# Kernel optimization log

Hardware: AMD Instinct MI355X
Metric: run time of the kernel (lower is better)

Reference implementation:

```python
import jax, jax.numpy as jnp
import numpy as np

B, G, C = 32, 50, 80
IMG = 640
STRIDES = (8, 16, 32)
CENTER_RADIUS = 2.5


def _make_grids():
    xs, ys, ss = [], [], []
    for s in STRIDES:
        n = IMG // s
        yv, xv = np.meshgrid(np.arange(n, dtype=np.float32), np.arange(n, dtype=np.float32), indexing='ij')
        xs.append(xv.reshape(-1)); ys.append(yv.reshape(-1))
        ss.append(np.full(n * n, s, dtype=np.float32))
    return np.concatenate(xs), np.concatenate(ys), np.concatenate(ss)


def setup_inputs():
    xg, yg, sg = _make_grids()
    A = xg.shape[0]  # 8400
    ks = jax.random.split(jax.random.key(0), 5)
    # decoded box predictions near grid centers (cxcywh, pixel units)
    ctr = jnp.stack([jnp.asarray((xg + 0.5) * sg), jnp.asarray((yg + 0.5) * sg)], -1)[None] \
        + jax.random.normal(ks[0], (B, A, 2)) * 8.0
    wh = jnp.exp(jax.random.normal(ks[1], (B, A, 2)) * 0.5) * jnp.asarray(sg)[None, :, None] * 4.0
    pred_output = jnp.concatenate([ctr, wh, jax.random.normal(ks[2], (B, A, 1 + C))], -1)  # [B,A,85]
    obj_preds = jax.random.normal(ks[3], (B, A, 1))
    cls_preds = jax.random.normal(ks[4], (B, A, C))
    # labels [B,G,5] = (class, cx, cy, w, h); first num_gt rows valid, rest zero
    rng = np.random.RandomState(0)
    lab = np.zeros((B, G, 5), np.float32)
    for b in range(B):
        ng = rng.randint(5, G)
        lab[b, :ng, 0] = rng.randint(0, C, ng)
        lab[b, :ng, 1:3] = rng.uniform(40.0, IMG - 40.0, (ng, 2))
        lab[b, :ng, 3:5] = rng.uniform(20.0, 160.0, (ng, 2))
    return {"pred_output": pred_output, "obj_preds": obj_preds, "cls_preds": cls_preds,
            "labels": jnp.asarray(lab), "x_shifts": jnp.asarray(xg),
            "y_shifts": jnp.asarray(yg), "strides": jnp.asarray(sg)}


def _pairwise_iou_cxcywh(a, b):
    # a [G,4], b [A,4] -> [G,A]
    tl = jnp.maximum(a[:, None, :2] - a[:, None, 2:] * 0.5, b[None, :, :2] - b[None, :, 2:] * 0.5)
    br = jnp.minimum(a[:, None, :2] + a[:, None, 2:] * 0.5, b[None, :, :2] + b[None, :, 2:] * 0.5)
    area_a = a[:, 2] * a[:, 3]
    area_b = b[:, 2] * b[:, 3]
    en = jnp.all(tl < br, -1).astype(a.dtype)
    area_i = jnp.prod(br - tl, -1) * en
    return area_i / (area_a[:, None] + area_b[None, :] - area_i + 1e-16)


def _assign_one(gt, gt_valid, boxes, cls_logit, obj_logit, xg, yg, sg):
    # SimOTA assignment for a single image, fully vectorized over [G,A].
    # gt [G,5], gt_valid [G], boxes [A,4], cls_logit [A,C], obj_logit [A,1]
    num_gt = gt.shape[0]
    gt_cls = gt[:, 0].astype(jnp.int32)
    gb = gt[:, 1:5]
    xc = (xg + 0.5) * sg
    yc = (yg + 0.5) * sg
    d_box = jnp.stack([
        xc[None, :] - (gb[:, 0:1] - gb[:, 2:3] * 0.5),
        (gb[:, 0:1] + gb[:, 2:3] * 0.5) - xc[None, :],
        yc[None, :] - (gb[:, 1:2] - gb[:, 3:4] * 0.5),
        (gb[:, 1:2] + gb[:, 3:4] * 0.5) - yc[None, :]], -1)
    in_boxes = (jnp.min(d_box, -1) > 0) & gt_valid[:, None]
    d_ctr = jnp.stack([
        xc[None, :] - (gb[:, 0:1] - CENTER_RADIUS * sg[None, :]),
        (gb[:, 0:1] + CENTER_RADIUS * sg[None, :]) - xc[None, :],
        yc[None, :] - (gb[:, 1:2] - CENTER_RADIUS * sg[None, :]),
        (gb[:, 1:2] + CENTER_RADIUS * sg[None, :]) - yc[None, :]], -1)
    in_ctr = (jnp.min(d_ctr, -1) > 0) & gt_valid[:, None]
    fg0 = jnp.any(in_boxes | in_ctr, 0)           # [A] candidate anchors (fg_mask)
    and_ctr = in_boxes & in_ctr                    # [G,A]
    ious = _pairwise_iou_cxcywh(gb, boxes) * fg0[None, :].astype(boxes.dtype) * gt_valid[:, None].astype(boxes.dtype)
    # pairwise BCE(sqrt(sig(cls)*sig(obj)), one_hot) summed over classes, without [G,A,C]
    logq = 0.5 * (jax.nn.log_sigmoid(cls_logit) + jax.nn.log_sigmoid(obj_logit))  # [A,C]
    q = jnp.clip(jnp.exp(logq), 1e-7, 1.0 - 1e-7)
    s_neg = jnp.sum(jnp.log1p(-q), -1)             # [A] sum_c log(1-q_c)
    q_gt = q[:, gt_cls].T                          # [G,A]
    cls_cost = -jnp.log(q_gt) + jnp.log1p(-q_gt) - s_neg[None, :]
    invalid = (~fg0)[None, :] | (~gt_valid)[:, None]
    cost = cls_cost - 3.0 * jnp.log(ious + 1e-8) + 1e5 * (~and_ctr) + 1e9 * invalid
    # dynamic-k: sum of top-10 ious per gt, truncated, min 1
    dyn_k = jnp.maximum(jnp.sum(jax.lax.top_k(ious, 10)[0], -1).astype(jnp.int32), 1)  # [G]
    ranks = jnp.argsort(jnp.argsort(cost, 1), 1)   # rank of each anchor in ascending cost
    matching = (ranks < dyn_k[:, None]) & gt_valid[:, None]
    # resolve anchors claimed by >1 gt: keep min-cost gt
    best_gt = jnp.argmin(cost, 0)                  # [A]
    onehot_best = jnp.arange(num_gt)[:, None] == best_gt[None, :]
    matching = jnp.where(jnp.sum(matching, 0)[None, :] > 1, onehot_best, matching)
    fg = jnp.any(matching, 0)                      # [A] final fg mask
    matched = jnp.argmax(matching, 0)              # [A] matched gt index
    pred_iou = jnp.sum(matching * ious, 0)         # [A]
    cls_t = jax.nn.one_hot(gt_cls[matched], cls_logit.shape[-1], dtype=boxes.dtype) \
        * (pred_iou * fg.astype(boxes.dtype))[:, None]
    return cls_t, fg, matched


def _forward(pred_output, obj_preds, cls_preds, labels, x_shifts, y_shifts, strides):
    bbox = pred_output[:, :, :4]
    gt_valid = labels.sum(-1) > 0
    cls_t, fg, matched = jax.vmap(_assign_one, in_axes=(0, 0, 0, 0, 0, None, None, None))(
        labels, gt_valid, bbox, cls_preds, obj_preds, x_shifts, y_shifts, strides)
    cls_t = jax.lax.stop_gradient(cls_t)  # get_assignments is @torch.no_grad()
    reg_t = jnp.take_along_axis(labels[:, :, 1:5], matched[:, :, None], axis=1)  # [B,A,4]
    fg_f = fg.astype(pred_output.dtype)
    num_fg = jnp.maximum(jnp.sum(fg_f), 1.0)
    # IoU loss (cxcywh), loss = 1 - iou^2, only on fg anchors
    tl = jnp.maximum(bbox[..., :2] - bbox[..., 2:] * 0.5, reg_t[..., :2] - reg_t[..., 2:] * 0.5)
    br = jnp.minimum(bbox[..., :2] + bbox[..., 2:] * 0.5, reg_t[..., :2] + reg_t[..., 2:] * 0.5)
    en = jnp.all(tl < br, -1).astype(bbox.dtype)
    area_i = jnp.prod(br - tl, -1) * en
    area_u = bbox[..., 2] * bbox[..., 3] + reg_t[..., 2] * reg_t[..., 3] - area_i
    iou = area_i / (area_u + 1e-16)
    loss_iou = jnp.sum((1.0 - iou ** 2) * fg_f) / num_fg
    bce = lambda x, y: jax.nn.softplus(x) - x * y  # BCEWithLogits, reduction='none'
    loss_obj = jnp.sum(bce(obj_preds[..., 0], fg_f)) / num_fg
    loss_cls = jnp.sum(bce(cls_preds, cls_t) * fg_f[..., None]) / num_fg
    return 5.0 * loss_iou + loss_obj + loss_cls


def reference(pred_output, obj_preds, cls_preds, labels, x_shifts, y_shifts, strides):
    return _forward(pred_output, obj_preds, cls_preds, labels, x_shifts, y_shifts, strides)
```

## Files before the change

### kernel.cpp

```cpp
#include <hip/hip_runtime.h>
#include <cstdint>
#include <cstddef>

#define BB 32
#define GG 50
#define CC 80
#define AA 8400
#define PCH (5 + CC)
#define NLB ((BB * AA + 255) / 256)
#define NXCD 8
#define FGBIT 63
#define SENTC 3.3e38f
#define SENTI 0x7fffffff

__device__ __forceinline__ float logsig_fast(float x) {
    float e = __expf(-fabsf(x));
    return fminf(x, 0.f) - __logf(1.f + e);
}
__device__ __forceinline__ void sp_ls(float x, float& sp, float& ls) {
    float e = __expf(-fabsf(x));
    float l = __logf(1.f + e);
    sp = fmaxf(x, 0.f) + l;
    ls = fminf(x, 0.f) - l;
}
__device__ __forceinline__ float softplusf(float x) {
    return fmaxf(x, 0.f) + log1pf(expf(-fabsf(x)));
}

__device__ __forceinline__ float pair_iou(float px, float py, float pw, float ph,
                                          float gx, float gy, float gw, float gh) {
    float tlx = fmaxf(gx - gw * 0.5f, px - pw * 0.5f);
    float tly = fmaxf(gy - gh * 0.5f, py - ph * 0.5f);
    float brx = fminf(gx + gw * 0.5f, px + pw * 0.5f);
    float bry = fminf(gy + gh * 0.5f, py + ph * 0.5f);
    float en = (tlx < brx && tly < bry) ? 1.f : 0.f;
    float ai = (brx - tlx) * (bry - tly) * en;
    return ai / (gw * gh + pw * ph - ai + 1e-16f);
}
__device__ __forceinline__ float cost_val(float x , float lo ,
                                          float sn , float v ,
                                          bool ac, bool f0, bool valid) {
    float lq = 0.5f * (logsig_fast(x) + lo);
    float q = fminf(fmaxf(__expf(lq), 1e-7f), 1.f - 1e-7f);
    float cst = -__logf(q) + __logf(1.f - q) - sn;
    cst -= 3.0f * __logf(v + 1e-8f);
    cst += 100000.0f * (ac ? 0.f : 1.f);
    cst += 1000000000.0f * ((!f0 || !valid) ? 1.f : 0.f);
    return cst;
}

__global__ __launch_bounds__(256)
void k_precompute(const float* __restrict__ pred, const float* __restrict__ obj,
                  const float* __restrict__ cls,
                  float2* __restrict__ lsn, float* __restrict__ sps,
                  float4* __restrict__ pbox) {
    int t = blockIdx.x * blockDim.x + threadIdx.x;
    int i = t >> 2;
    int sub = t & 3;
    if (i >= BB * AA) return;
    float lo = logsig_fast(obj[i]);
    const float4* c4 = (const float4*)(cls + (size_t)i * CC);
    float sn = 0.f, sp = 0.f;
#pragma unroll
    for (int j = 0; j < 5; j++) {
        float4 v = c4[sub + 4 * j];
        float xs4[4] = {v.x, v.y, v.z, v.w};
#pragma unroll
        for (int u = 0; u < 4; u++) {
            float x = xs4[u];
            float spx, lsx;
            sp_ls(x, spx, lsx);
            sp += spx;
            float q = __expf(0.5f * (lsx + lo));
            q = fminf(fmaxf(q, 1e-7f), 1.f - 1e-7f);
            sn += __logf(1.f - q);
        }
    }
    sp += __shfl_xor(sp, 1); sn += __shfl_xor(sn, 1);
    sp += __shfl_xor(sp, 2); sn += __shfl_xor(sn, 2);
    float pv = pred[(size_t)i * PCH + sub];
    ((float*)pbox)[(size_t)i * 4 + sub] = pv;
    if (sub == 0) {
        lsn[i] = make_float2(lo, sn);
        sps[i] = sp;
    }
}

__global__ void k_geom(const float* __restrict__ labels, const float* __restrict__ xs,
                       const float* __restrict__ ys, const float* __restrict__ ss,
                       unsigned long long* __restrict__ amask,
                       int* __restrict__ clist, int* __restrict__ ccnt) {
    int b = blockIdx.y;
    int a = blockIdx.x * blockDim.x + threadIdx.x;
    __shared__ float lab[GG * 5];
    __shared__ int lv[GG];
    for (int t = threadIdx.x; t < GG * 5; t += blockDim.x) lab[t] = labels[b * GG * 5 + t];
    __syncthreads();
    if (threadIdx.x < GG) {
        const float* r = lab + threadIdx.x * 5;
        lv[threadIdx.x] = ((r[0] + r[1] + r[2] + r[3] + r[4]) > 0.f) ? 1 : 0;
    }
    __syncthreads();
    if (a >= AA) return;
    float s = ss[a];
    float xc = (xs[a] + 0.5f) * s;
    float yc = (ys[a] + 0.5f) * s;
    unsigned long long m = 0;
    int any = 0;
    for (int g = 0; g < GG; g++) {
        if (!lv[g]) continue;
        const float* r = lab + g * 5;
        float gx = r[1], gy = r[2], gw = r[3], gh = r[4];
        float d1 = xc - (gx - gw * 0.5f);
        float d2 = (gx + gw * 0.5f) - xc;
        float d3 = yc - (gy - gh * 0.5f);
        float d4 = (gy + gh * 0.5f) - yc;
        bool ib = fminf(fminf(d1, d2), fminf(d3, d4)) > 0.f;
        float cr = 2.5f * s;
        float e1 = xc - (gx - cr);
        float e2 = (gx + cr) - xc;
        float e3 = yc - (gy - cr);
        float e4 = (gy + cr) - yc;
        bool ic = fminf(fminf(e1, e2), fminf(e3, e4)) > 0.f;
        if (ib || ic) any = 1;
        if (ib && ic) m |= 1ull << g;
    }
    if (any) m |= 1ull << FGBIT;
    amask[b * AA + a] = m;
    int lane = threadIdx.x & 63;
    unsigned long long act = __ballot(m != 0);
    if (act) {
        int leader = __ffsll(act) - 1;
        int base = 0;
        if (lane == leader) base = atomicAdd(&ccnt[b], __popcll(act));
        base = __shfl(base, leader);
        if (m != 0) {
            int off = __popcll(act & ((1ull << lane) - 1ull));
            clist[b * AA + base + off] = a;
        }
    }
}

__global__ __launch_bounds__(256)
void k_assign(const float4* __restrict__ pbox, const float2* __restrict__ lsn,
              const float* __restrict__ cls,
              const unsigned long long* __restrict__ amask,
              const float* __restrict__ labels,
              const int* __restrict__ clist, const int* __restrict__ ccnt,
              unsigned long long* __restrict__ mmask) {
    int bid = blockIdx.x;
    int w = (bid % NXCD) * (BB * GG / NXCD) + bid / NXCD;
    int b = w / GG, g = w % GG;
    const float* r = labels + (size_t)w * 5;
    float gcls = r[0], gx = r[1], gy = r[2], gw = r[3], gh = r[4];
    if (!((gcls + gx + gy + gw + gh) > 0.f)) return;
    int gtc = (int)gcls;
    int tid = threadIdx.x;
    int lane = tid & 63;
    int wv = tid >> 6;
    int cnt = ccnt[b];

    float ivl[10];
    float cvl[10];
    int   cil[10];
#pragma unroll
    for (int t = 0; t < 10; t++) { ivl[t] = 0.f; cvl[t] = SENTC; cil[t] = SENTI; }
    int nac = 0;

    for (int i0 = wv * 64; i0 < cnt; i0 += 256) {
        int i = i0 + lane;
        bool inr = i < cnt;
        int a = clist[b * AA + (inr ? i : (cnt - 1))];
        int ia = b * AA + a;
        unsigned long long am = amask[ia];
        float4 pb = pbox[ia];
        bool f0 = inr && ((am >> FGBIT) & 1ull);
        bool ac = inr && ((am >> g) & 1ull);
        nac += __popcll(__ballot(ac));
        float v = f0 ? pair_iou(pb.x, pb.y, pb.z, pb.w, gx, gy, gw, gh) : 0.f;
        {
            float mv = v;
            while (true) {
                unsigned long long mb = __ballot(mv > ivl[9]);
                if (!mb) break;
                int src = __ffsll(mb) - 1;
                float bv = __shfl(mv, src);
#pragma unroll
                for (int t = 0; t < 10; t++)
                    if (bv > ivl[t]) { float tmp = ivl[t]; ivl[t] = bv; bv = tmp; }
                if (lane == src) mv = -1.f;
            }
        }
        {
            float c = SENTC; int id = SENTI;
            if (ac) {
                float x = cls[(size_t)ia * CC + gtc];
                float2 ls = lsn[ia];
                c = cost_val(x, ls.x, ls.y, v, true, true, true);
                id = a;
            }
            while (true) {
                bool enter = (c < cvl[9]) || (c == cvl[9] && id < cil[9]);
                unsigned long long mb = __ballot(enter);
                if (!mb) break;
                int src = __ffsll(mb) - 1;
                float bc = __shfl(c, src);
                int bi = __shfl(id, src);
#pragma unroll
                for (int t = 0; t < 10; t++) {
                    bool sw = (bc < cvl[t]) || (bc == cvl[t] && bi < cil[t]);
                    if (sw) {
                        float tf = cvl[t]; cvl[t] = bc; bc = tf;
                        int ti = cil[t]; cil[t] = bi; bi = ti;
                    }
                }
                if (lane == src) { c = SENTC; id = SENTI; }
            }
        }
    }

    __shared__ float IV[4][10];
    __shared__ float CV[4][10];
    __shared__ int CI[4][10];
    __shared__ int NAC[4];
    __shared__ int s_k, s_n0;
    __shared__ int sel[10];

    if (lane == 0) {
#pragma unroll
        for (int t = 0; t < 10; t++) { IV[wv][t] = ivl[t]; CV[wv][t] = cvl[t]; CI[wv][t] = cil[t]; }
        NAC[wv] = nac;
    }
    __syncthreads();
    if (tid == 0) {
        int h[4] = {0, 0, 0, 0};
        float ssum = 0.f;
        for (int j = 0; j < 10; j++) {
            float bv = -1.f; int bc = 0;
#pragma unroll
            for (int c2 = 0; c2 < 4; c2++)
                if (h[c2] < 10 && IV[c2][h[c2]] > bv) { bv = IV[c2][h[c2]]; bc = c2; }
            ssum += bv;
            h[bc]++;
        }
        int k = (int)ssum;
        if (k < 1) k = 1;
        s_k = k;
        s_n0 = NAC[0] + NAC[1] + NAC[2] + NAC[3];
    }
    __syncthreads();
    int k = s_k;

    if (s_n0 < k) {
        const int chunk = AA / 4;
        int abase = wv * chunk, aend = abase + chunk;
#pragma unroll
        for (int t = 0; t < 10; t++) { cvl[t] = SENTC; cil[t] = SENTI; }
        for (int a0 = abase; a0 < aend; a0 += 64) {
            int a = a0 + lane;
            bool inr = a < aend;
            int ia = b * AA + (inr ? a : (aend - 1));
            unsigned long long am = amask[ia];
            bool f0 = inr && ((am >> FGBIT) & 1ull);
            bool ac = inr && ((am >> g) & 1ull);
            float v = 0.f;
            if (f0) {
                float4 pb = pbox[ia];
                v = pair_iou(pb.x, pb.y, pb.z, pb.w, gx, gy, gw, gh);
            }
            float c = SENTC; int id = SENTI;
            if (inr) {
                float x = cls[(size_t)ia * CC + gtc];
                float2 ls = lsn[ia];
                c = cost_val(x, ls.x, ls.y, v, ac, f0, true);
                id = a;
            }
            while (true) {
                bool enter = (c < cvl[9]) || (c == cvl[9] && id < cil[9]);
                unsigned long long mb = __ballot(enter);
                if (!mb) break;
                int src = __ffsll(mb) - 1;
                float bc = __shfl(c, src);
                int bi = __shfl(id, src);
#pragma unroll
                for (int t = 0; t < 10; t++) {
                    bool sw = (bc < cvl[t]) || (bc == cvl[t] && bi < cil[t]);
                    if (sw) {
                        float tf = cvl[t]; cvl[t] = bc; bc = tf;
                        int ti = cil[t]; cil[t] = bi; bi = ti;
                    }
                }
                if (lane == src) { c = SENTC; id = SENTI; }
            }
        }
        if (lane == 0) {
#pragma unroll
            for (int t = 0; t < 10; t++) { CV[wv][t] = cvl[t]; CI[wv][t] = cil[t]; }
        }
        __syncthreads();
    }

    if (tid == 0) {
        int h[4] = {0, 0, 0, 0};
        for (int j = 0; j < k; j++) {
            float bv = SENTC; int bix = SENTI; int bc = 0;
#pragma unroll
            for (int c2 = 0; c2 < 4; c2++) {
                if (h[c2] < 10) {
                    float av = CV[c2][h[c2]]; int ax = CI[c2][h[c2]];
                    if (av < bv || (av == bv && ax < bix)) { bv = av; bix = ax; bc = c2; }
                }
            }
            sel[j] = bix;
            h[bc]++;
        }
    }
    __syncthreads();
    if (tid < k) {
        atomicOr(&mmask[(size_t)b * AA + sel[tid]], 1ull << g);
    }
}

__global__ void k_loss(const float4* __restrict__ pbox, const float* __restrict__ obj,
                       const float* __restrict__ cls, const float* __restrict__ labels,
                       const float2* __restrict__ lsn,
                       const unsigned long long* __restrict__ amask,
                       const unsigned long long* __restrict__ mmask,
                       const float* __restrict__ sps, float* __restrict__ partial) {
    int i = blockIdx.x * blockDim.x + threadIdx.x;
    float li = 0.f, lo = 0.f, lc = 0.f, nf = 0.f;
    if (i < BB * AA) {
        int b = i / AA, a = i % AA;
        unsigned long long m = mmask[i];
        int cnt = __popcll(m);
        bool fg = (m != 0);
        int mg = 0;
        float4 pb = pbox[i];
        unsigned long long am = amask[i];
        bool f0 = (am >> FGBIT) & 1ull;
        if (cnt > 1) {
            float2 ls = lsn[i];
            float bv = 3.4e38f;
            for (int g = 0; g < GG; g++) {
                const float* r = labels + (size_t)(b * GG + g) * 5;
                float gcls = r[0], gx = r[1], gy = r[2], gw = r[3], gh = r[4];
                bool valid = (gcls + gx + gy + gw + gh) > 0.f;
                int gtc = (int)gcls;
                float raw = pair_iou(pb.x, pb.y, pb.z, pb.w, gx, gy, gw, gh);
                float v = raw * (f0 ? 1.f : 0.f) * (valid ? 1.f : 0.f);
                float x = cls[(size_t)i * CC + gtc];
                bool ac = (am >> g) & 1ull;
                float cst = cost_val(x, ls.x, ls.y, v, ac, f0, valid);
                if (cst < bv) { bv = cst; mg = g; }
            }
        } else if (cnt == 1) {
            mg = __ffsll((unsigned long long)m) - 1;
        }
        float o = obj[i];
        lo = softplusf(o) - (fg ? o : 0.f);
        if (fg) {
            const float* r = labels + (size_t)(b * GG + mg) * 5;
            float gcls = r[0], gx = r[1], gy = r[2], gw = r[3], gh = r[4];
            bool valid = (gcls + gx + gy + gw + gh) > 0.f;
            int gtc = (int)gcls;
            float piou = pair_iou(pb.x, pb.y, pb.z, pb.w, gx, gy, gw, gh)
                         * (f0 ? 1.f : 0.f) * (valid ? 1.f : 0.f);
            float tlx = fmaxf(pb.x - pb.z * 0.5f, gx - gw * 0.5f);
            float tly = fmaxf(pb.y - pb.w * 0.5f, gy - gh * 0.5f);
            float brx = fminf(pb.x + pb.z * 0.5f, gx + gw * 0.5f);
            float bry = fminf(pb.y + pb.w * 0.5f, gy + gh * 0.5f);
            float en = (tlx < brx && tly < bry) ? 1.f : 0.f;
            float ai = (brx - tlx) * (bry - tly) * en;
            float u = pb.z * pb.w + gw * gh - ai;
            float v2 = ai / (u + 1e-16f);
            li = 1.f - v2 * v2;
            lc = sps[i] - cls[(size_t)i * CC + gtc] * piou;
            nf = 1.f;
        }
    }
    for (int off = 32; off; off >>= 1) {
        li += __shfl_down(li, off);
        lo += __shfl_down(lo, off);
        lc += __shfl_down(lc, off);
        nf += __shfl_down(nf, off);
    }
    __shared__ float red[4][4];
    int wid = threadIdx.x >> 6;
    if ((threadIdx.x & 63) == 0) {
        red[wid][0] = li; red[wid][1] = lo; red[wid][2] = lc; red[wid][3] = nf;
    }
    __syncthreads();
    if (threadIdx.x == 0) {
        float s0 = 0.f, s1 = 0.f, s2 = 0.f, s3 = 0.f;
#pragma unroll
        for (int t = 0; t < 4; t++) {
            s0 += red[t][0]; s1 += red[t][1]; s2 += red[t][2]; s3 += red[t][3];
        }
        float4* pb = (float4*)partial;
        pb[blockIdx.x] = make_float4(s0, s1, s2, s3);
    }
}

__global__ void k_final(const float* __restrict__ partial, float* __restrict__ out) {
    int tid = threadIdx.x;
    float s0 = 0.f, s1 = 0.f, s2 = 0.f, s3 = 0.f;
    const float4* pb = (const float4*)partial;
    for (int i = tid; i < NLB; i += 256) {
        float4 v = pb[i];
        s0 += v.x; s1 += v.y; s2 += v.z; s3 += v.w;
    }
    for (int off = 32; off; off >>= 1) {
        s0 += __shfl_down(s0, off);
        s1 += __shfl_down(s1, off);
        s2 += __shfl_down(s2, off);
        s3 += __shfl_down(s3, off);
    }
    __shared__ float red[4][4];
    int wid = tid >> 6;
    if ((tid & 63) == 0) {
        red[wid][0] = s0; red[wid][1] = s1; red[wid][2] = s2; red[wid][3] = s3;
    }
    __syncthreads();
    if (tid == 0) {
        float li = 0.f, lo = 0.f, lc = 0.f, nf = 0.f;
#pragma unroll
        for (int t = 0; t < 4; t++) {
            li += red[t][0]; lo += red[t][1]; lc += red[t][2]; nf += red[t][3];
        }
        nf = fmaxf(nf, 1.f);
        out[0] = (5.f * li + lo + lc) / nf;
    }
}

extern "C" void kernel_launch(void* const* d_in, const int* in_sizes, int n_in,
                              void* d_out, int out_size, void* d_ws, size_t ws_size,
                              hipStream_t stream) {
    const float* pred = (const float*)d_in[0];
    const float* obj  = (const float*)d_in[1];
    const float* cls  = (const float*)d_in[2];
    const float* lab  = (const float*)d_in[3];
    const float* xs   = (const float*)d_in[4];
    const float* ys   = (const float*)d_in[5];
    const float* ss   = (const float*)d_in[6];
    float* out = (float*)d_out;

    const size_t BA = (size_t)BB * AA;

    float2* lsn  = (float2*)d_ws;
    float*  sps  = (float*)(lsn + BA);
    float4* pbox = (float4*)(sps + BA);
    unsigned long long* amask = (unsigned long long*)(pbox + BA);
    unsigned long long* mmask = amask + BA;
    float* partial = (float*)(mmask + BA);
    int* clist = (int*)(partial + (size_t)NLB * 4);
    int* ccnt  = clist + BA;

    hipMemsetAsync(mmask, 0, BA * sizeof(unsigned long long), stream);
    hipMemsetAsync(ccnt, 0, BB * sizeof(int), stream);

    dim3 blk(256);
    k_precompute<<<dim3((BB * AA * 4 + 255) / 256), blk, 0, stream>>>(pred, obj, cls,
                                                                      lsn, sps, pbox);
    k_geom<<<dim3((AA + 255) / 256, BB), blk, 0, stream>>>(lab, xs, ys, ss, amask,
                                                           clist, ccnt);
    k_assign<<<dim3(BB * GG), blk, 0, stream>>>(pbox, lsn, cls, amask, lab,
                                                clist, ccnt, mmask);
    k_loss<<<dim3(NLB), blk, 0, stream>>>(pbox, obj, cls, lab, lsn, amask,
                                          mmask, sps, partial);
    k_final<<<1, blk, 0, stream>>>(partial, out);
}
```

Measured before the change: 177.6 us.

## Replace per-element transcendental calls with product-of-terms logs in precompute

```diff
diff --git a/kernel.cpp b/kernel.cpp
--- a/kernel.cpp
+++ b/kernel.cpp
@@ -8,7 +8,6 @@
 #define AA 8400
 #define PCH (5 + CC)
 #define NLB ((BB * AA + 255) / 256)
-#define NXCD 8
 #define FGBIT 63
 #define SENTC 3.3e38f
 #define SENTI 0x7fffffff
@@ -16,12 +15,6 @@
 __device__ __forceinline__ float logsig_fast(float x) {
     float e = __expf(-fabsf(x));
     return fminf(x, 0.f) - __logf(1.f + e);
-}
-__device__ __forceinline__ void sp_ls(float x, float& sp, float& ls) {
-    float e = __expf(-fabsf(x));
-    float l = __logf(1.f + e);
-    sp = fmaxf(x, 0.f) + l;
-    ls = fminf(x, 0.f) - l;
 }
 __device__ __forceinline__ float softplusf(float x) {
     return fmaxf(x, 0.f) + log1pf(expf(-fabsf(x)));
@@ -59,23 +52,29 @@
     int sub = t & 3;
     if (i >= BB * AA) return;
     float lo = logsig_fast(obj[i]);
+    float K = __expf(0.5f * lo);
     const float4* c4 = (const float4*)(cls + (size_t)i * CC);
-    float sn = 0.f, sp = 0.f;
+    float smax = 0.f, psp = 1.f, p1 = 1.f, p2 = 1.f;
 #pragma unroll
     for (int j = 0; j < 5; j++) {
         float4 v = c4[sub + 4 * j];
         float xs4[4] = {v.x, v.y, v.z, v.w};
+        float pg = 1.f;
 #pragma unroll
         for (int u = 0; u < 4; u++) {
             float x = xs4[u];
-            float spx, lsx;
-            sp_ls(x, spx, lsx);
-            sp += spx;
-            float q = __expf(0.5f * (lsx + lo));
-            q = fminf(fmaxf(q, 1e-7f), 1.f - 1e-7f);
-            sn += __logf(1.f - q);
-        }
-    }
+            float th = __expf(-0.5f * fabsf(x));
+            float t2 = th * th;
+            smax += fmaxf(x, 0.f);
+            psp *= (1.f + t2);
+            float qq = K * (x < 0.f ? th : 1.f) * rsqrtf(1.f + t2);
+            qq = fminf(fmaxf(qq, 1e-7f), 1.f - 1e-7f);
+            pg *= (1.f - qq);
+        }
+        if (j < 2) p1 *= pg; else p2 *= pg;
+    }
+    float sp = smax + __logf(psp);
+    float sn = __logf(p1) + __logf(p2);
     sp += __shfl_xor(sp, 1); sn += __shfl_xor(sn, 1);
     sp += __shfl_xor(sp, 2); sn += __shfl_xor(sn, 2);
     float pv = pred[(size_t)i * PCH + sub];
@@ -148,8 +147,7 @@
               const float* __restrict__ labels,
               const int* __restrict__ clist, const int* __restrict__ ccnt,
               unsigned long long* __restrict__ mmask) {
-    int bid = blockIdx.x;
-    int w = (bid % NXCD) * (BB * GG / NXCD) + bid / NXCD;
+    int w = blockIdx.x;
     int b = w / GG, g = w % GG;
     const float* r = labels + (size_t)w * 5;
     float gcls = r[0], gx = r[1], gy = r[2], gw = r[3], gh = r[4];
```

Measured after the change: 170.1 us. -4.3%, faster.
